# Kernel optimization log

Hardware: AMD Instinct MI355X
Metric: run time of the kernel (lower is better)

## Reference

```python
import jax, jax.numpy as jnp
import numpy as np

B, N, C = 8, 8192, 64
NPOINT = 2048
RADIUS = 0.2
NSAMPLE = 32


def _fps_single(xyz, npoint):
    # xyz: (N, 3). Iterative farthest point sampling, start at index 0.
    n = xyz.shape[0]

    def body(carry, _):
        min_d, last = carry
        d = jnp.sum((xyz - xyz[last]) ** 2, axis=-1)   # (N,)
        min_d = jnp.minimum(min_d, d)
        nxt = jnp.argmax(min_d).astype(jnp.int32)
        return (min_d, nxt), nxt

    init = (jnp.full((n,), jnp.inf, xyz.dtype), jnp.int32(0))
    _, idx = jax.lax.scan(body, init, None, length=npoint - 1)
    return jnp.concatenate([jnp.zeros((1,), jnp.int32), idx])  # (npoint,)


def _ball_query(xyz, new_xyz, radius, nsample):
    # xyz: (B, N, 3), new_xyz: (B, S, 3) -> neighbor idx (B, S, nsample)
    n = xyz.shape[1]
    # squared pairwise distances (B, S, N)
    d2 = (jnp.sum(new_xyz ** 2, -1)[:, :, None]
          + jnp.sum(xyz ** 2, -1)[:, None, :]
          - 2.0 * jnp.einsum('bsc,bnc->bsn', new_xyz, xyz))
    mask = d2 < radius * radius
    # valid indices first, in original order; invalid -> sentinel n
    key = jnp.where(mask, jnp.arange(n, dtype=jnp.int32)[None, None, :], n)
    srt = jnp.sort(key, axis=-1)[:, :, :nsample]      # (B, S, nsample)
    first = srt[:, :, :1]                             # pad with first valid (query itself)
    return jnp.where(srt >= n, first, srt).astype(jnp.int32)


def setup_inputs() -> dict:
    key = jax.random.key(0)
    k = jax.random.split(key, 8)
    s1 = 1.0 / np.sqrt(67.0)
    s2 = 1.0 / np.sqrt(64.0)
    return {
        'xyz': jax.random.uniform(k[0], (B, N, 3), jnp.float32),
        'features': jax.random.normal(k[1], (B, C, N), jnp.float32),
        'W1': jax.random.normal(k[2], (67, 64), jnp.float32) * s1,
        'b1': jnp.zeros((64,), jnp.float32),
        'W2': jax.random.normal(k[3], (64, 64), jnp.float32) * s2,
        'b2': jnp.zeros((64,), jnp.float32),
        'W3': jax.random.normal(k[4], (64, 128), jnp.float32) * s2,
        'b3': jnp.zeros((128,), jnp.float32),
    }


def reference(xyz, features, W1, b1, W2, b2, W3, b3):
    # 1) farthest point sampling -> centroid indices (B, S)
    fps_idx = jax.vmap(_fps_single, in_axes=(0, None))(xyz, NPOINT)
    new_xyz = jnp.take_along_axis(xyz, fps_idx[:, :, None], axis=1)  # (B, S, 3)

    # 2) ball query grouping
    idx = _ball_query(xyz, new_xyz, RADIUS, NSAMPLE)                 # (B, S, K)
    grouped_xyz = jnp.take_along_axis(
        xyz[:, None, :, :], idx[:, :, :, None], axis=2)              # (B, S, K, 3)
    grouped_xyz = grouped_xyz - new_xyz[:, :, None, :]               # relative coords
    feats_n = jnp.transpose(features, (0, 2, 1))                     # (B, N, C)
    grouped_feats = jnp.take_along_axis(
        feats_n[:, None, :, :], idx[:, :, :, None], axis=2)          # (B, S, K, C)
    g = jnp.concatenate([grouped_xyz, grouped_feats], axis=-1)       # (B, S, K, 3+C)

    # 3) shared MLP (1x1 conv2d equivalent) + ReLU
    h = jax.nn.relu(jnp.einsum('bskc,cd->bskd', g, W1) + b1)
    h = jax.nn.relu(jnp.einsum('bskc,cd->bskd', h, W2) + b2)
    h = jax.nn.relu(jnp.einsum('bskc,cd->bskd', h, W3) + b3)         # (B, S, K, 128)

    # 4) max-pool over the neighbor axis
    new_features = jnp.max(h, axis=2)                                # (B, S, 128)
    new_features = jnp.transpose(new_features, (0, 2, 1))            # (B, 128, S)
    return new_xyz, new_features
```

## Files before the change

### kernel.cpp

```cpp
#include <hip/hip_runtime.h>
#include <cstddef>

#define BATCH 8
#define NPTS 8192
#define NFEAT 64
#define NPOINT 2048
#define NSAMPLE 32

__device__ __forceinline__ float sq_nc(float a) {
    float r = a * a;
    asm volatile("" : "+v"(r));
    return r;
}
__device__ __forceinline__ float mul_nc(float a, float b) {
    float r = a * b;
    asm volatile("" : "+v"(r));
    return r;
}

__global__ __launch_bounds__(512) void fps_kernel(const float* __restrict__ xyz,
                                                  float* __restrict__ newxyz) {
    extern __shared__ float4 sp[];
    __shared__ alignas(16) unsigned long long redp[2][8];

    const int b = blockIdx.x;
    const int tid = threadIdx.x;
    const int lane = tid & 63;
    const int wid = tid >> 6;
    const float* xb = xyz + (size_t)b * NPTS * 3;

    for (int i = tid; i < NPTS; i += 512)
        sp[i] = make_float4(xb[i * 3 + 0], xb[i * 3 + 1], xb[i * 3 + 2], 0.0f);
    __syncthreads();

    float mx[16], my_[16], mz[16], md[16];
    const int base = tid * 16;
#pragma unroll
    for (int j = 0; j < 16; ++j) {
        float4 p = sp[base + j];
        mx[j] = p.x; my_[j] = p.y; mz[j] = p.z;
        md[j] = INFINITY;
    }

    float4 c0 = sp[0];
    if (tid == 0) {
        newxyz[(size_t)b * NPOINT * 3 + 0] = c0.x;
        newxyz[(size_t)b * NPOINT * 3 + 1] = c0.y;
        newxyz[(size_t)b * NPOINT * 3 + 2] = c0.z;
    }
    float xl = c0.x, yl = c0.y, zl = c0.z;
    int par = 0;

    for (int it = 1; it < NPOINT; ++it) {
        float bv = -1.0f;
        int bi = 0;
#pragma unroll
        for (int j = 0; j < 16; ++j) {
            float dx = mx[j] - xl;
            float dy = my_[j] - yl;
            float dz = mz[j] - zl;
            float d = (sq_nc(dx) + sq_nc(dy)) + sq_nc(dz);
            float m = fminf(md[j], d);
            md[j] = m;
            if (m > bv) { bv = m; bi = base + j; }
        }

        float wv = bv;
#pragma unroll
        for (int m = 1; m < 64; m <<= 1)
            wv = fmaxf(wv, __shfl_xor(wv, m, 64));
        unsigned long long msk = __ballot(bv == wv);
        int src = __builtin_ctzll(msk);
        int wbi = __shfl(bi, src, 64);

        if (lane == 0)
            redp[par][wid] = ((unsigned long long)__float_as_uint(wv) << 32) |
                             (unsigned int)(~(unsigned int)wbi);
        __syncthreads();

        const ulonglong2* rp = (const ulonglong2*)redp[par];
        ulonglong2 r0 = rp[0], r1 = rp[1], r2 = rp[2], r3 = rp[3];
        unsigned long long m0 = (r0.x > r0.y) ? r0.x : r0.y;
        unsigned long long m1 = (r1.x > r1.y) ? r1.x : r1.y;
        unsigned long long m2 = (r2.x > r2.y) ? r2.x : r2.y;
        unsigned long long m3 = (r3.x > r3.y) ? r3.x : r3.y;
        m0 = (m1 > m0) ? m1 : m0;
        m2 = (m3 > m2) ? m3 : m2;
        m0 = (m2 > m0) ? m2 : m0;
        const int fi = (int)(~(unsigned int)m0);

        float4 cc = sp[fi];
        xl = cc.x; yl = cc.y; zl = cc.z;
        if (tid == 0) {
            size_t o = (size_t)b * NPOINT * 3 + (size_t)it * 3;
            newxyz[o + 0] = xl;
            newxyz[o + 1] = yl;
            newxyz[o + 2] = zl;
        }
        par ^= 1;
    }
}

__global__ __launch_bounds__(64) void ball_kernel(const float* __restrict__ xyz,
                                                  const float* __restrict__ newxyz,
                                                  int* __restrict__ ballidx) {
    extern __shared__ float4 s4[];
    const int b = blockIdx.y;
    const int s = blockIdx.x * 64 + threadIdx.x;
    const float* xb = xyz + (size_t)b * NPTS * 3;
    for (int i = threadIdx.x; i < NPTS; i += 64) {
        float x = xb[i * 3 + 0], y = xb[i * 3 + 1], z = xb[i * 3 + 2];
        float sq = (sq_nc(x) + sq_nc(y)) + sq_nc(z);
        s4[i] = make_float4(x, y, z, sq);
    }
    __syncthreads();

    const int sIdx = b * NPOINT + s;
    float cx = newxyz[(size_t)sIdx * 3 + 0];
    float cy = newxyz[(size_t)sIdx * 3 + 1];
    float cz = newxyz[(size_t)sIdx * 3 + 2];
    float cq = (sq_nc(cx) + sq_nc(cy)) + sq_nc(cz);

    int* ob = ballidx + (size_t)sIdx * NSAMPLE;
    int cnt = 0;
    int first = 0;
#pragma unroll 4
    for (int n = 0; n < NPTS; ++n) {
        float4 p = s4[n];
        float dot = __fmaf_rn(cz, p.z, __fmaf_rn(cy, p.y, __fmul_rn(cx, p.x)));
        float d2 = (cq + p.w) - mul_nc(2.0f, dot);
        if (d2 < 0.04f && cnt < NSAMPLE) {
            ob[cnt] = n;
            if (cnt == 0) first = n;
            ++cnt;
        }
    }
    for (int j = cnt; j < NSAMPLE; ++j) ob[j] = first;
}

__global__ __launch_bounds__(256) void f1_kernel(const float* __restrict__ features,
                                                 const float* __restrict__ W1,
                                                 float* __restrict__ F1) {
    const int lane = threadIdx.x & 63;
    const int chunk = threadIdx.x >> 6;
    const int blk = blockIdx.x;
    const int b = blk >> 7;
    const int n = ((blk & 127) << 6) | lane;
    const float* fb = features + (size_t)b * NFEAT * NPTS + n;
    const float* wbase = W1 + 3 * 64 + chunk * 16;

    float acc[16];
#pragma unroll
    for (int i = 0; i < 16; ++i) acc[i] = 0.0f;

#pragma unroll 4
    for (int cp = 0; cp < 64; ++cp) {
        float f = fb[(size_t)cp * NPTS];
        const float4* w = reinterpret_cast<const float4*>(wbase + (size_t)cp * 64);
#pragma unroll
        for (int c4 = 0; c4 < 4; ++c4) {
            float4 ww = w[c4];
            acc[c4 * 4 + 0] += f * ww.x;
            acc[c4 * 4 + 1] += f * ww.y;
            acc[c4 * 4 + 2] += f * ww.z;
            acc[c4 * 4 + 3] += f * ww.w;
        }
    }
    float* o = F1 + ((size_t)b * NPTS + n) * 64 + chunk * 16;
#pragma unroll
    for (int c4 = 0; c4 < 4; ++c4) {
        float4 v;
        v.x = acc[c4 * 4 + 0]; v.y = acc[c4 * 4 + 1];
        v.z = acc[c4 * 4 + 2]; v.w = acc[c4 * 4 + 3];
        *reinterpret_cast<float4*>(o + c4 * 4) = v;
    }
}

__global__ __launch_bounds__(256) void mlp_kernel(const float* __restrict__ xyz,
                                                  const float* __restrict__ W1,
                                                  const float* __restrict__ b1,
                                                  const float* __restrict__ W2,
                                                  const float* __restrict__ b2,
                                                  const float* __restrict__ W3,
                                                  const float* __restrict__ b3,
                                                  const float* __restrict__ F1,
                                                  const int* __restrict__ ballidx,
                                                  const float* __restrict__ newxyz,
                                                  float* __restrict__ outF) {
    __shared__ float hbuf[64][256];
    const int tid = threadIdx.x;
    const int k = tid & 31;
    const int sIdx = blockIdx.x * 8 + (tid >> 5);
    const int b = sIdx >> 11;
    const int s = sIdx & (NPOINT - 1);

    const int p = ballidx[(size_t)sIdx * NSAMPLE + k];
    const float* xb = xyz + (size_t)b * NPTS * 3;
    float rx = xb[p * 3 + 0] - newxyz[(size_t)sIdx * 3 + 0];
    float ry = xb[p * 3 + 1] - newxyz[(size_t)sIdx * 3 + 1];
    float rz = xb[p * 3 + 2] - newxyz[(size_t)sIdx * 3 + 2];

    const float* f1p = F1 + ((size_t)b * NPTS + p) * 64;
#pragma unroll 4
    for (int c4 = 0; c4 < 16; ++c4) {
        float4 f  = *reinterpret_cast<const float4*>(f1p + c4 * 4);
        float4 wx = *reinterpret_cast<const float4*>(W1 + c4 * 4);
        float4 wy = *reinterpret_cast<const float4*>(W1 + 64 + c4 * 4);
        float4 wz = *reinterpret_cast<const float4*>(W1 + 128 + c4 * 4);
        float4 bb = *reinterpret_cast<const float4*>(b1 + c4 * 4);
        hbuf[c4 * 4 + 0][tid] = fmaxf(bb.x + f.x + rx * wx.x + ry * wy.x + rz * wz.x, 0.0f);
        hbuf[c4 * 4 + 1][tid] = fmaxf(bb.y + f.y + rx * wx.y + ry * wy.y + rz * wz.y, 0.0f);
        hbuf[c4 * 4 + 2][tid] = fmaxf(bb.z + f.z + rx * wx.z + ry * wy.z + rz * wz.z, 0.0f);
        hbuf[c4 * 4 + 3][tid] = fmaxf(bb.w + f.w + rx * wx.w + ry * wy.w + rz * wz.w, 0.0f);
    }

    float h2[64];
#pragma unroll
    for (int d4 = 0; d4 < 16; ++d4) {
        float4 bb = *reinterpret_cast<const float4*>(b2 + d4 * 4);
        h2[d4 * 4 + 0] = bb.x; h2[d4 * 4 + 1] = bb.y;
        h2[d4 * 4 + 2] = bb.z; h2[d4 * 4 + 3] = bb.w;
    }
#pragma unroll 4
    for (int c = 0; c < 64; ++c) {
        float a = hbuf[c][tid];
        const float4* w = reinterpret_cast<const float4*>(W2 + (size_t)c * 64);
#pragma unroll
        for (int d4 = 0; d4 < 16; ++d4) {
            float4 ww = w[d4];
            h2[d4 * 4 + 0] += a * ww.x;
            h2[d4 * 4 + 1] += a * ww.y;
            h2[d4 * 4 + 2] += a * ww.z;
            h2[d4 * 4 + 3] += a * ww.w;
        }
    }
#pragma unroll
    for (int d = 0; d < 64; ++d) hbuf[d][tid] = fmaxf(h2[d], 0.0f);

    const size_t obase = (size_t)b * 128 * NPOINT + s;
#pragma unroll 1
    for (int ch = 0; ch < 4; ++ch) {
        float acc[32];
#pragma unroll
        for (int j4 = 0; j4 < 8; ++j4) {
            float4 bb = *reinterpret_cast<const float4*>(b3 + ch * 32 + j4 * 4);
            acc[j4 * 4 + 0] = bb.x; acc[j4 * 4 + 1] = bb.y;
            acc[j4 * 4 + 2] = bb.z; acc[j4 * 4 + 3] = bb.w;
        }
#pragma unroll 4
        for (int c = 0; c < 64; ++c) {
            float a = hbuf[c][tid];
            const float4* w = reinterpret_cast<const float4*>(W3 + (size_t)c * 128 + ch * 32);
#pragma unroll
            for (int j4 = 0; j4 < 8; ++j4) {
                float4 ww = w[j4];
                acc[j4 * 4 + 0] += a * ww.x;
                acc[j4 * 4 + 1] += a * ww.y;
                acc[j4 * 4 + 2] += a * ww.z;
                acc[j4 * 4 + 3] += a * ww.w;
            }
        }
#pragma unroll
        for (int j = 0; j < 32; ++j) {
            float v = fmaxf(acc[j], 0.0f);
#pragma unroll
            for (int m = 16; m >= 1; m >>= 1) v = fmaxf(v, __shfl_xor(v, m, 64));
            acc[j] = v;
        }
        if (k == 0) {
#pragma unroll
            for (int j = 0; j < 32; ++j)
                outF[obase + (size_t)(ch * 32 + j) * NPOINT] = acc[j];
        }
    }
}

extern "C" void kernel_launch(void* const* d_in, const int* in_sizes, int n_in,
                              void* d_out, int out_size, void* d_ws, size_t ws_size,
                              hipStream_t stream) {
    const float* xyz      = (const float*)d_in[0];
    const float* features = (const float*)d_in[1];
    const float* W1       = (const float*)d_in[2];
    const float* b1       = (const float*)d_in[3];
    const float* W2       = (const float*)d_in[4];
    const float* b2       = (const float*)d_in[5];
    const float* W3       = (const float*)d_in[6];
    const float* b3       = (const float*)d_in[7];

    float* out_newxyz = (float*)d_out;
    float* out_feat   = (float*)d_out + (size_t)BATCH * NPOINT * 3;

    int*   ballidx = (int*)d_ws;
    float* F1      = (float*)((char*)d_ws + (size_t)BATCH * NPOINT * NSAMPLE * 4);

    f1_kernel<<<1024, 256, 0, stream>>>(features, W1, F1);

    fps_kernel<<<BATCH, 512, NPTS * 16, stream>>>(xyz, out_newxyz);

    ball_kernel<<<dim3(NPOINT / 64, BATCH), 64, NPTS * 16, stream>>>(xyz, out_newxyz, ballidx);

    mlp_kernel<<<(BATCH * NPOINT) / 8, 256, 0, stream>>>(
        xyz, W1, b1, W2, b2, W3, b3, F1, ballidx, out_newxyz, out_feat);
}
```

Measured before the change: 2.868 ms.

## Merge FPS and feature projection into one launch to overlap them

Fuses the f1 feature-projection kernel into the FPS kernel as extra blocks, so the serial 8-block FPS runs concurrently with the 512 projection blocks instead of after them. FPS shared memory changes from a float4 array to three separate x/y/z arrays, which cuts LDS use from 128KB to 96KB per block. Projection blocks now reserve the same dynamic LDS and 512 threads, which may limit their occupancy, and block scheduling order decides whether FPS blocks start early.

```diff
diff --git a/kernel.cpp b/kernel.cpp
--- a/kernel.cpp
+++ b/kernel.cpp
@@ -18,37 +18,85 @@
     return r;
 }
 
-__global__ __launch_bounds__(512) void fps_kernel(const float* __restrict__ xyz,
-                                                  float* __restrict__ newxyz) {
-    extern __shared__ float4 sp[];
+__global__ __launch_bounds__(512) void fps_f1_kernel(const float* __restrict__ xyz,
+                                                     const float* __restrict__ features,
+                                                     const float* __restrict__ W1,
+                                                     float* __restrict__ F1,
+                                                     float* __restrict__ newxyz) {
+    extern __shared__ float lds[];
+    const int tid = threadIdx.x;
+
+    if (blockIdx.x >= 8) {
+        const int lane = tid & 63;
+        const int chunk = (tid >> 6) & 3;
+        const int sub = tid >> 8;
+        const int fblk = blockIdx.x - 8;
+        const int b = fblk >> 6;
+        const int n = ((fblk & 63) << 7) + (sub << 6) + lane;
+        const float* fb = features + (size_t)b * NFEAT * NPTS + n;
+        const float* wbase = W1 + 3 * 64 + chunk * 16;
+
+        float acc[16];
+#pragma unroll
+        for (int i = 0; i < 16; ++i) acc[i] = 0.0f;
+
+#pragma unroll 4
+        for (int cp = 0; cp < 64; ++cp) {
+            float f = fb[(size_t)cp * NPTS];
+            const float4* w = reinterpret_cast<const float4*>(wbase + (size_t)cp * 64);
+#pragma unroll
+            for (int c4 = 0; c4 < 4; ++c4) {
+                float4 ww = w[c4];
+                acc[c4 * 4 + 0] += f * ww.x;
+                acc[c4 * 4 + 1] += f * ww.y;
+                acc[c4 * 4 + 2] += f * ww.z;
+                acc[c4 * 4 + 3] += f * ww.w;
+            }
+        }
+        float* o = F1 + ((size_t)b * NPTS + n) * 64 + chunk * 16;
+#pragma unroll
+        for (int c4 = 0; c4 < 4; ++c4) {
+            float4 v;
+            v.x = acc[c4 * 4 + 0]; v.y = acc[c4 * 4 + 1];
+            v.z = acc[c4 * 4 + 2]; v.w = acc[c4 * 4 + 3];
+            *reinterpret_cast<float4*>(o + c4 * 4) = v;
+        }
+        return;
+    }
+
+    float* sx = lds;
+    float* sy = lds + NPTS;
+    float* sz = lds + 2 * NPTS;
     __shared__ alignas(16) unsigned long long redp[2][8];
 
     const int b = blockIdx.x;
-    const int tid = threadIdx.x;
     const int lane = tid & 63;
     const int wid = tid >> 6;
     const float* xb = xyz + (size_t)b * NPTS * 3;
 
-    for (int i = tid; i < NPTS; i += 512)
-        sp[i] = make_float4(xb[i * 3 + 0], xb[i * 3 + 1], xb[i * 3 + 2], 0.0f);
+    for (int i = tid; i < NPTS; i += 512) {
+        sx[i] = xb[i * 3 + 0];
+        sy[i] = xb[i * 3 + 1];
+        sz[i] = xb[i * 3 + 2];
+    }
     __syncthreads();
 
     float mx[16], my_[16], mz[16], md[16];
     const int base = tid * 16;
 #pragma unroll
     for (int j = 0; j < 16; ++j) {
-        float4 p = sp[base + j];
-        mx[j] = p.x; my_[j] = p.y; mz[j] = p.z;
+        mx[j] = sx[base + j];
+        my_[j] = sy[base + j];
+        mz[j] = sz[base + j];
         md[j] = INFINITY;
     }
 
-    float4 c0 = sp[0];
     if (tid == 0) {
-        newxyz[(size_t)b * NPOINT * 3 + 0] = c0.x;
-        newxyz[(size_t)b * NPOINT * 3 + 1] = c0.y;
-        newxyz[(size_t)b * NPOINT * 3 + 2] = c0.z;
-    }
-    float xl = c0.x, yl = c0.y, zl = c0.z;
+        newxyz[(size_t)b * NPOINT * 3 + 0] = sx[0];
+        newxyz[(size_t)b * NPOINT * 3 + 1] = sy[0];
+        newxyz[(size_t)b * NPOINT * 3 + 2] = sz[0];
+    }
+    float xl = sx[0], yl = sy[0], zl = sz[0];
     int par = 0;
 
     for (int it = 1; it < NPOINT; ++it) {
@@ -89,8 +137,7 @@
         m0 = (m2 > m0) ? m2 : m0;
         const int fi = (int)(~(unsigned int)m0);
 
-        float4 cc = sp[fi];
-        xl = cc.x; yl = cc.y; zl = cc.z;
+        xl = sx[fi]; yl = sy[fi]; zl = sz[fi];
         if (tid == 0) {
             size_t o = (size_t)b * NPOINT * 3 + (size_t)it * 3;
             newxyz[o + 0] = xl;
@@ -136,44 +183,6 @@
         }
     }
     for (int j = cnt; j < NSAMPLE; ++j) ob[j] = first;
-}
-
-__global__ __launch_bounds__(256) void f1_kernel(const float* __restrict__ features,
-                                                 const float* __restrict__ W1,
-                                                 float* __restrict__ F1) {
-    const int lane = threadIdx.x & 63;
-    const int chunk = threadIdx.x >> 6;
-    const int blk = blockIdx.x;
-    const int b = blk >> 7;
-    const int n = ((blk & 127) << 6) | lane;
-    const float* fb = features + (size_t)b * NFEAT * NPTS + n;
-    const float* wbase = W1 + 3 * 64 + chunk * 16;
-
-    float acc[16];
-#pragma unroll
-    for (int i = 0; i < 16; ++i) acc[i] = 0.0f;
-
-#pragma unroll 4
-    for (int cp = 0; cp < 64; ++cp) {
-        float f = fb[(size_t)cp * NPTS];
-        const float4* w = reinterpret_cast<const float4*>(wbase + (size_t)cp * 64);
-#pragma unroll
-        for (int c4 = 0; c4 < 4; ++c4) {
-            float4 ww = w[c4];
-            acc[c4 * 4 + 0] += f * ww.x;
-            acc[c4 * 4 + 1] += f * ww.y;
-            acc[c4 * 4 + 2] += f * ww.z;
-            acc[c4 * 4 + 3] += f * ww.w;
-        }
-    }
-    float* o = F1 + ((size_t)b * NPTS + n) * 64 + chunk * 16;
-#pragma unroll
-    for (int c4 = 0; c4 < 4; ++c4) {
-        float4 v;
-        v.x = acc[c4 * 4 + 0]; v.y = acc[c4 * 4 + 1];
-        v.z = acc[c4 * 4 + 2]; v.w = acc[c4 * 4 + 3];
-        *reinterpret_cast<float4*>(o + c4 * 4) = v;
-    }
 }
 
 __global__ __launch_bounds__(256) void mlp_kernel(const float* __restrict__ xyz,
@@ -293,9 +302,7 @@
     int*   ballidx = (int*)d_ws;
     float* F1      = (float*)((char*)d_ws + (size_t)BATCH * NPOINT * NSAMPLE * 4);
 
-    f1_kernel<<<1024, 256, 0, stream>>>(features, W1, F1);
-
-    fps_kernel<<<BATCH, 512, NPTS * 16, stream>>>(xyz, out_newxyz);
+    fps_f1_kernel<<<8 + 512, 512, 3 * NPTS * 4, stream>>>(xyz, features, W1, F1, out_newxyz);
 
     ball_kernel<<<dim3(NPOINT / 64, BATCH), 64, NPTS * 16, stream>>>(xyz, out_newxyz, ballidx);
 
```

Result: faster. 2.780 ms (-3.1%).
